# Optimization experiments

Measured on AMD Instinct MI355X. Metric: run time of the kernel, lower is better.

## Reference

```python
import jax, jax.numpy as jnp
import numpy as np

S, B, H, NH = 2048, 4, 1024, 16
HD = H // NH
MASK_VAL = -10000.0

def setup_inputs() -> dict:
    key = jax.random.key(0)
    ks = jax.random.split(key, 6)
    hidden_states = jax.random.normal(ks[0], (S, B, H), dtype=jnp.float32)
    attention_mask = jax.random.randint(ks[1], (B, 1, S, S), 0, 2).astype(bool)
    W_qkv = jax.random.normal(ks[2], (3 * H, H), dtype=jnp.float32) * (H ** -0.5)
    b_qkv = jax.random.normal(ks[3], (3 * H,), dtype=jnp.float32) * 0.02
    W_dense = jax.random.normal(ks[4], (H, H), dtype=jnp.float32) * (H ** -0.5)
    b_dense = jax.random.normal(ks[5], (H,), dtype=jnp.float32) * 0.02
    return {"hidden_states": hidden_states, "attention_mask": attention_mask,
            "W_qkv": W_qkv, "b_qkv": b_qkv, "W_dense": W_dense, "b_dense": b_dense}

def reference(hidden_states, attention_mask, W_qkv, b_qkv, W_dense, b_dense):
    # QKV projection: [s,b,h] -> [s,b,3h] -> [s,b,NH,3*HD], split last dim into q,k,v
    mixed = hidden_states @ W_qkv.T + b_qkv
    mixed = mixed.reshape(S, B, NH, 3 * HD)
    q, k, v = mixed[..., :HD], mixed[..., HD:2 * HD], mixed[..., 2 * HD:]
    norm_factor = jnp.float32(1.0 / np.sqrt(HD))
    # scores: [b, nh, sq, sk] (baddbmm beta=0.7 on torch.empty is undefined; baseline treated as 0)
    scores = jnp.einsum('sbhd,tbhd->bhst', q, k) * norm_factor
    scores = jnp.where(attention_mask, MASK_VAL, scores)
    probs = jax.nn.softmax(scores, axis=-1)
    # attention dropout (p=0.7) omitted for deterministic reference (eval mode)
    ctx = jnp.einsum('bhst,tbhd->sbhd', probs, v)  # [s,b,nh,hd]
    ctx = ctx.reshape(S, B, H)
    out = ctx @ W_dense.T + b_dense
    return out
```

## Files before the change

kernel.cpp:

```cpp
#include <hip/hip_runtime.h>
#include <hip/hip_bf16.h>
#include <math.h>

constexpr int S_ = 2048, B_ = 4, H_ = 1024, NH_ = 16, HD_ = 64;

typedef __attribute__((ext_vector_type(8))) short short8;
typedef __attribute__((ext_vector_type(4))) short short4v;
typedef __attribute__((ext_vector_type(4))) float floatx4;
typedef __attribute__((ext_vector_type(2))) unsigned uint2v;

static __device__ __forceinline__ short f2bf(float f) {
    union { float f; unsigned u; } v; v.f = f;
    unsigned r = v.u + 0x7FFFu + ((v.u >> 16) & 1u);
    return (short)(r >> 16);
}

static __device__ __forceinline__ unsigned pack_bf(float p0, float p1) {
    return __builtin_amdgcn_perm(__float_as_uint(p1), __float_as_uint(p0), 0x07060302u);
}
static __device__ __forceinline__ float bfl(unsigned u) { return __uint_as_float(u << 16); }
static __device__ __forceinline__ float bfh(unsigned u) { return __uint_as_float(u & 0xFFFF0000u); }

static __device__ __forceinline__ void gl2lds16(const void* g, void* l) {
    __builtin_amdgcn_global_load_lds(
        (const __attribute__((address_space(1))) void*)g,
        (__attribute__((address_space(3))) void*)l, 16, 0, 0);
}

static __device__ __forceinline__ short8 pswz(unsigned a0, unsigned a1,
                                              unsigned b0, unsigned b1) {
    uint2v r0 = __builtin_amdgcn_permlane32_swap(a0, b0, false, false);
    uint2v s0 = __builtin_amdgcn_permlane16_swap(r0.x, r0.y, false, false);
    uint2v r1 = __builtin_amdgcn_permlane32_swap(a1, b1, false, false);
    uint2v s1 = __builtin_amdgcn_permlane16_swap(r1.x, r1.y, false, false);
    union { unsigned u[4]; short8 s; } o;
    o.u[0] = s0.x;
    o.u[1] = s1.x;
    o.u[2] = s0.y;
    o.u[3] = s1.y;
    return o.s;
}

__global__ __launch_bounds__(256) void cvt3_kernel(
    const float* __restrict__ a, short* __restrict__ oa, int na,
    const float* __restrict__ b, short* __restrict__ ob, int nb,
    const float* __restrict__ c, short* __restrict__ oc, int nc)
{
    const int idx = blockIdx.x * 256 + threadIdx.x;
    const float* src; short* dst; int i;
    if (idx < na)            { src = a; dst = oa; i = idx; }
    else if (idx < na + nb)  { src = b; dst = ob; i = idx - na; }
    else                     { src = c; dst = oc; i = idx - na - nb; }
    const float4 v = ((const float4*)src)[i];
    short4v o = { (short)f2bf(v.x), (short)f2bf(v.y), (short)f2bf(v.z), (short)f2bf(v.w) };
    ((short4v*)dst)[i] = o;
}

__global__ __launch_bounds__(256) void mask_u8_kernel(
    const int* __restrict__ m, unsigned* __restrict__ mb)
{
    const int i = blockIdx.x * 256 + threadIdx.x;
    const int4 v = ((const int4*)m)[i];
    unsigned r = (v.x ? 0u : 0xFFu)      | (v.y ? 0u : 0xFF00u) |
                 (v.z ? 0u : 0xFF0000u)  | (v.w ? 0u : 0xFF000000u);
    mb[i] = r;
}

__global__ __launch_bounds__(256) void gemm_qkv_mfma(
    const short* __restrict__ A, const short* __restrict__ Bw,
    const float* __restrict__ bias,
    short* __restrict__ Qb, short* __restrict__ Kb, short* __restrict__ Vb)
{
    constexpr int K = H_;
    __shared__ __align__(16) short As[128 * 64];
    __shared__ __align__(16) short Bs[128 * 64];

    const int t = threadIdx.x;
    const int wave = t >> 6, lane = t & 63;
    const int l15 = lane & 15, quad = lane >> 4;
    const int wm = wave & 1, wn = wave >> 1;
    const int row0 = blockIdx.y * 128;
    const int col0 = blockIdx.x * 128;

    floatx4 acc[4][4];
#pragma unroll
    for (int mi = 0; mi < 4; ++mi)
#pragma unroll
        for (int ni = 0; ni < 4; ++ni)
            acc[mi][ni] = (floatx4){0.f, 0.f, 0.f, 0.f};

    for (int k0 = 0; k0 < K; k0 += 64) {
#pragma unroll
        for (int j = 0; j < 4; ++j) {
            const int c = wave * 256 + j * 64 + lane;
            const int r = c >> 3, jg = ((c & 7) ^ (r & 7)) * 8;
            gl2lds16(A  + (size_t)(row0 + r) * K + k0 + jg, &As[(wave * 256 + j * 64) * 8]);
            gl2lds16(Bw + (size_t)(col0 + r) * K + k0 + jg, &Bs[(wave * 256 + j * 64) * 8]);
        }
        __syncthreads();
#pragma unroll
        for (int kk = 0; kk < 64; kk += 32) {
            short8 af[4], bfr[4];
#pragma unroll
            for (int mi = 0; mi < 4; ++mi) {
                const int R = wm * 64 + mi * 16 + l15;
                af[mi] = *(const short8*)&As[R * 64 + ((((kk >> 3) + quad) ^ (R & 7)) * 8)];
            }
#pragma unroll
            for (int ni = 0; ni < 4; ++ni) {
                const int R = wn * 64 + ni * 16 + l15;
                bfr[ni] = *(const short8*)&Bs[R * 64 + ((((kk >> 3) + quad) ^ (R & 7)) * 8)];
            }
#pragma unroll
            for (int mi = 0; mi < 4; ++mi)
#pragma unroll
                for (int ni = 0; ni < 4; ++ni)
                    acc[mi][ni] = __builtin_amdgcn_mfma_f32_16x16x32_bf16(
                        af[mi], bfr[ni], acc[mi][ni], 0, 0, 0);
        }
        __syncthreads();
    }

#pragma unroll
    for (int ni = 0; ni < 4; ++ni) {
        const int gc = col0 + wn * 64 + ni * 16 + l15;
        const float bv = bias[gc];
        const int hh = gc / 192;
        const int rem = gc - hh * 192;
        const int which = rem >> 6, d = rem & 63;
#pragma unroll
        for (int mi = 0; mi < 4; ++mi)
#pragma unroll
            for (int i = 0; i < 4; ++i) {
                const int gr = row0 + wm * 64 + mi * 16 + quad * 4 + i;
                const int s = gr >> 2, bb = gr & 3;
                float fv = acc[mi][ni][i] + bv;
                const size_t ho = (size_t)(bb * NH_ + hh);
                if (which == 0)      Qb[(ho * S_ + s) * HD_ + d] = f2bf(fv * 0.1803368801111204f);
                else if (which == 1) Kb[(ho * S_ + s) * HD_ + d] = f2bf(fv);
                else                 Vb[(ho * S_ + s) * HD_ + d] = f2bf(fv);
            }
    }
}

__global__ __launch_bounds__(256) void vtrans_kernel(
    const short* __restrict__ Vb, short* __restrict__ Vtb)
{
    const int bh = blockIdx.y;
    const int s0 = blockIdx.x * 64;
    __shared__ __align__(16) short T[64 * 64];
    const int t = threadIdx.x;

#pragma unroll
    for (int it = 0; it < 2; ++it) {
        const int c = t + it * 256;
        const int r = c >> 3, jp = c & 7;
        const int jg = jp ^ ((r >> 3) & 7);
        *(short8*)&T[r * 64 + jp * 8] =
            *(const short8*)(Vb + ((size_t)bh * S_ + s0 + r) * HD_ + jg * 8);
    }
    __syncthreads();

#pragma unroll
    for (int it = 0; it < 2; ++it) {
        const int c = t + it * 256;
        const int d = c >> 3, sg = (c & 7) * 8;
        short8 v;
#pragma unroll
        for (int k = 0; k < 8; ++k) {
            const int r = sg + k;
            v[k] = T[r * 64 + (((d >> 3) ^ ((r >> 3) & 7)) * 8) + (d & 7)];
        }
        *(short8*)(Vtb + ((size_t)bh * HD_ + d) * S_ + s0 + sg) = v;
    }
}

__global__ __launch_bounds__(256) void gemm_dense_mfma(
    const short* __restrict__ A, const short* __restrict__ Bw,
    const float* __restrict__ bias, float* __restrict__ out)
{
    constexpr int K = H_;
    __shared__ __align__(16) short As[128 * 64];
    __shared__ __align__(16) short Bs[128 * 64];

    const int t = threadIdx.x;
    const int wave = t >> 6, lane = t & 63;
    const int l15 = lane & 15, quad = lane >> 4;
    const int wm = wave & 1, wn = wave >> 1;
    const int row0 = blockIdx.y * 128;
    const int col0 = blockIdx.x * 128;

    floatx4 acc[4][4];
#pragma unroll
    for (int mi = 0; mi < 4; ++mi)
#pragma unroll
        for (int ni = 0; ni < 4; ++ni)
            acc[mi][ni] = (floatx4){0.f, 0.f, 0.f, 0.f};

    for (int k0 = 0; k0 < K; k0 += 64) {
#pragma unroll
        for (int j = 0; j < 4; ++j) {
            const int c = wave * 256 + j * 64 + lane;
            const int r = c >> 3, jg = ((c & 7) ^ (r & 7)) * 8;
            gl2lds16(A  + (size_t)(row0 + r) * K + k0 + jg, &As[(wave * 256 + j * 64) * 8]);
            gl2lds16(Bw + (size_t)(col0 + r) * K + k0 + jg, &Bs[(wave * 256 + j * 64) * 8]);
        }
        __syncthreads();
#pragma unroll
        for (int kk = 0; kk < 64; kk += 32) {
            short8 af[4], bfr[4];
#pragma unroll
            for (int mi = 0; mi < 4; ++mi) {
                const int R = wm * 64 + mi * 16 + l15;
                af[mi] = *(const short8*)&As[R * 64 + ((((kk >> 3) + quad) ^ (R & 7)) * 8)];
            }
#pragma unroll
            for (int ni = 0; ni < 4; ++ni) {
                const int R = wn * 64 + ni * 16 + l15;
                bfr[ni] = *(const short8*)&Bs[R * 64 + ((((kk >> 3) + quad) ^ (R & 7)) * 8)];
            }
#pragma unroll
            for (int mi = 0; mi < 4; ++mi)
#pragma unroll
                for (int ni = 0; ni < 4; ++ni)
                    acc[mi][ni] = __builtin_amdgcn_mfma_f32_16x16x32_bf16(
                        af[mi], bfr[ni], acc[mi][ni], 0, 0, 0);
        }
        __syncthreads();
    }

#pragma unroll
    for (int ni = 0; ni < 4; ++ni) {
        const int gc = col0 + wn * 64 + ni * 16 + l15;
        const float bv = bias[gc];
#pragma unroll
        for (int mi = 0; mi < 4; ++mi)
#pragma unroll
            for (int i = 0; i < 4; ++i) {
                const int gr = row0 + wm * 64 + mi * 16 + quad * 4 + i;
                out[(size_t)gr * H_ + gc] = acc[mi][ni][i] + bv;
            }
    }
}

__global__ __launch_bounds__(256, 2) void flash_mfma_kernel(
    const short* __restrict__ Qb, const short* __restrict__ Kb,
    const short* __restrict__ Vtb, const unsigned char* __restrict__ mask8,
    short* __restrict__ ctxb)
{
    const int bh = blockIdx.y;
    const int b  = bh >> 4;
    const int h  = bh & 15;
    const int s0 = blockIdx.x * 256;

    const int tdx  = threadIdx.x;
    const int wave = tdx >> 6;
    const int lane = tdx & 63;
    const int l15  = lane & 15;
    const int quad = lane >> 4;

    __shared__ __align__(16) short Ks [3 * 4096];
    __shared__ __align__(16) short Vts[3 * 4096];

    const short* Qg = Qb + ((size_t)bh * S_ + s0 + wave * 64 + l15) * HD_;
    short8 qf[4][2];
#pragma unroll
    for (int g = 0; g < 4; ++g) {
        qf[g][0] = *(const short8*)(Qg + g * 16 * HD_ + quad * 8);
        qf[g][1] = *(const short8*)(Qg + g * 16 * HD_ + 32 + quad * 8);
    }

    const short* Kbase  = Kb  + (size_t)bh * S_ * HD_;
    const short* Vtbase = Vtb + (size_t)bh * HD_ * S_;
    const unsigned char* mr = mask8 + ((size_t)b * S_ + s0 + wave * 64 + l15) * S_ + quad * 4;

    floatx4 o[4][4];
    float ls[4] = {0.f, 0.f, 0.f, 0.f};
#pragma unroll
    for (int g = 0; g < 4; ++g)
#pragma unroll
        for (int n0 = 0; n0 < 4; ++n0) o[g][n0] = (floatx4){0.f, 0.f, 0.f, 0.f};

    const int cb0 = wave * 64, cb1 = (4 + wave) * 64;
    const int c0 = cb0 + lane,  c1 = cb1 + lane;
    const int r0 = c0 >> 3, jg0 = ((c0 & 7) ^ (r0 & 7)) * 8;
    const int r1 = c1 >> 3, jg1 = ((c1 & 7) ^ (r1 & 7)) * 8;

    gl2lds16(Kbase  + (size_t)r0 * HD_ + jg0, &Ks[cb0 * 8]);
    gl2lds16(Kbase  + (size_t)r1 * HD_ + jg1, &Ks[cb1 * 8]);
    gl2lds16(Vtbase + (size_t)r0 * S_ + jg0,  &Vts[cb0 * 8]);
    gl2lds16(Vtbase + (size_t)r1 * S_ + jg1,  &Vts[cb1 * 8]);
    __builtin_amdgcn_sched_barrier(0);
    gl2lds16(Kbase  + (size_t)(64 + r0) * HD_ + jg0, &Ks[4096 + cb0 * 8]);
    gl2lds16(Kbase  + (size_t)(64 + r1) * HD_ + jg1, &Ks[4096 + cb1 * 8]);
    gl2lds16(Vtbase + (size_t)r0 * S_ + 64 + jg0,    &Vts[4096 + cb0 * 8]);
    gl2lds16(Vtbase + (size_t)r1 * S_ + 64 + jg1,    &Vts[4096 + cb1 * 8]);
    __builtin_amdgcn_sched_barrier(0);
    unsigned mu[4][4], mun[4][4];
#pragma unroll
    for (int g = 0; g < 4; ++g)
#pragma unroll
        for (int n0 = 0; n0 < 4; ++n0)
            mu[g][n0] = *(const unsigned*)(mr + (size_t)g * 16 * S_ + n0 * 16);

    const floatx4 z4 = {0.f, 0.f, 0.f, 0.f};
    int boC = 0, boS = 2 * 4096;

#pragma unroll 1
    for (int it = 0; it < 32; ++it) {
        if (it < 31) { asm volatile("s_waitcnt vmcnt(20)" ::: "memory"); }
        else         { asm volatile("s_waitcnt vmcnt(16)" ::: "memory"); }
        __builtin_amdgcn_s_barrier();
        __builtin_amdgcn_sched_barrier(0);

        if (it < 30) {
            const size_t tn = (size_t)(it + 2) * 64;
            gl2lds16(Kbase  + (tn + r0) * HD_ + jg0,      &Ks[boS + cb0 * 8]);
            gl2lds16(Kbase  + (tn + r1) * HD_ + jg1,      &Ks[boS + cb1 * 8]);
            gl2lds16(Vtbase + (size_t)r0 * S_ + tn + jg0, &Vts[boS + cb0 * 8]);
            gl2lds16(Vtbase + (size_t)r1 * S_ + tn + jg1, &Vts[boS + cb1 * 8]);
        }
        __builtin_amdgcn_sched_barrier(0);
        if (it < 31) {
            const int tn1 = (it + 1) * 64;
#pragma unroll
            for (int g = 0; g < 4; ++g)
#pragma unroll
                for (int n0 = 0; n0 < 4; ++n0)
                    mun[g][n0] = *(const unsigned*)(mr + (size_t)g * 16 * S_ + tn1 + n0 * 16);
        }
        __builtin_amdgcn_sched_barrier(0);

#pragma unroll
        for (int h2 = 0; h2 < 2; ++h2) {
            unsigned uu[4][2][2];
            __builtin_amdgcn_s_setprio(1);
#pragma unroll
            for (int n0i = 0; n0i < 2; ++n0i) {
                const int n0 = h2 * 2 + n0i;
                const int R = n0 * 16 + l15, xr = R & 7;
                const short8 kb0 = *(const short8*)&Ks[boC + R * 64 + ((quad ^ xr) * 8)];
                const short8 kb1 = *(const short8*)&Ks[boC + R * 64 + (((quad + 4) ^ xr) * 8)];
#pragma unroll
                for (int g = 0; g < 4; ++g) {
                    floatx4 sc = __builtin_amdgcn_mfma_f32_16x16x32_bf16(kb0, qf[g][0], z4, 0, 0, 0);
                    sc = __builtin_amdgcn_mfma_f32_16x16x32_bf16(kb1, qf[g][1], sc, 0, 0, 0);
                    const unsigned q0 = __builtin_amdgcn_perm(0u, mu[g][n0], 0x01010000u);
                    const unsigned q1 = __builtin_amdgcn_perm(0u, mu[g][n0], 0x03030202u);
                    const unsigned u0 = pack_bf(__builtin_amdgcn_exp2f(sc[0]),
                                                __builtin_amdgcn_exp2f(sc[1])) & q0;
                    const unsigned u1 = pack_bf(__builtin_amdgcn_exp2f(sc[2]),
                                                __builtin_amdgcn_exp2f(sc[3])) & q1;
                    ls[g] += (bfl(u0) + bfh(u0)) + (bfl(u1) + bfh(u1));
                    uu[g][n0i][0] = u0; uu[g][n0i][1] = u1;
                }
            }
            __builtin_amdgcn_s_setprio(0);
            short8 pa[4];
#pragma unroll
            for (int g = 0; g < 4; ++g)
                pa[g] = pswz(uu[g][0][0], uu[g][0][1], uu[g][1][0], uu[g][1][1]);
            __builtin_amdgcn_s_setprio(1);
#pragma unroll
            for (int n0 = 0; n0 < 4; ++n0) {
                const int R = n0 * 16 + l15, xr = R & 7;
                const short8 vb = *(const short8*)&Vts[boC + R * 64 + (((quad + 4 * h2) ^ xr) * 8)];
#pragma unroll
                for (int g = 0; g < 4; ++g)
                    o[g][n0] = __builtin_amdgcn_mfma_f32_16x16x32_bf16(pa[g], vb, o[g][n0], 0, 0, 0);
            }
            __builtin_amdgcn_s_setprio(0);
        }

        boC = (boC == 2 * 4096) ? 0 : boC + 4096;
        boS = (boS == 2 * 4096) ? 0 : boS + 4096;
#pragma unroll
        for (int g = 0; g < 4; ++g)
#pragma unroll
            for (int n0 = 0; n0 < 4; ++n0) mu[g][n0] = mun[g][n0];
    }

#pragma unroll
    for (int g = 0; g < 4; ++g) {
        float lg = ls[g];
        lg += __shfl_xor(lg, 16);
        lg += __shfl_xor(lg, 32);
        const float li = 1.f / lg;
#pragma unroll
        for (int i = 0; i < 4; ++i) {
            const float la = __shfl(li, quad * 4 + i);
            const int sA = s0 + wave * 64 + g * 16 + quad * 4 + i;
#pragma unroll
            for (int n0 = 0; n0 < 4; ++n0)
                ctxb[((size_t)sA * B_ + b) * H_ + h * HD_ + n0 * 16 + l15] =
                    f2bf(o[g][n0][i] * la);
        }
    }
}

extern "C" void kernel_launch(void* const* d_in, const int* in_sizes, int n_in,
                              void* d_out, int out_size, void* d_ws, size_t ws_size,
                              hipStream_t stream)
{
    const float* hidden = (const float*)d_in[0];
    const int*   mask   = (const int*)d_in[1];
    const float* Wqkv   = (const float*)d_in[2];
    const float* bqkv   = (const float*)d_in[3];
    const float* Wd     = (const float*)d_in[4];
    const float* bd     = (const float*)d_in[5];
    float* out = (float*)d_out;

    const size_t HE = (size_t)B_ * NH_ * S_ * HD_;
    short* hBF    = (short*)d_ws;
    short* WqkvBF = hBF + (size_t)S_ * B_ * H_;
    short* WdBF   = WqkvBF + (size_t)3 * H_ * H_;
    short* Qb     = WdBF + (size_t)H_ * H_;
    short* Kb     = Qb + HE;
    short* Vb     = Kb + HE;
    short* Vtb    = Vb + HE;
    short* ctxb   = Vtb + HE;
    unsigned char* mask8 = (unsigned char*)hBF;

    const int nh4 = (S_ * B_ * H_) / 4;
    const int nw4 = (3 * H_ * H_) / 4;
    const int nd4 = (H_ * H_) / 4;
    hipLaunchKernelGGL(cvt3_kernel, dim3((nh4 + nw4 + nd4) / 256), dim3(256), 0, stream,
                       hidden, hBF, nh4, Wqkv, WqkvBF, nw4, Wd, WdBF, nd4);

    hipLaunchKernelGGL(gemm_qkv_mfma, dim3((3 * H_) / 128, (S_ * B_) / 128), dim3(256), 0, stream,
                       hBF, WqkvBF, bqkv, Qb, Kb, Vb);
    hipLaunchKernelGGL(mask_u8_kernel, dim3((B_ * S_ * S_ / 4) / 256), dim3(256), 0, stream,
                       mask, (unsigned*)mask8);
    hipLaunchKernelGGL(vtrans_kernel, dim3(S_ / 64, B_ * NH_), dim3(256), 0, stream,
                       Vb, Vtb);
    hipLaunchKernelGGL(flash_mfma_kernel, dim3(S_ / 256, B_ * NH_), dim3(256), 0, stream,
                       Qb, Kb, Vtb, mask8, ctxb);
    hipLaunchKernelGGL(gemm_dense_mfma, dim3(H_ / 128, (S_ * B_) / 128), dim3(256), 0, stream,
                       ctxb, WdBF, bd, out);
}
```

Before: 404.4 us.

## Halve flash-attention query tile per block and double-buffer mask registers

The flash attention kernel now processes 128 query rows per block (32 per wave) instead of 256, doubling the grid to 1024 blocks and raising the launch-bounds occupancy target to 3 blocks per CU. The inner loop is restructured to compute all QK scores for a 64-key tile before exp/pack, and to use a full 64-wide K in the PV MFMAs. The loop is unrolled by two with ping-pong mask registers, which replaces the register copy, and the last tile is peeled. The aim is to fill CUs better and cut register pressure, at the cost of reloading K/V tiles from memory twice as often per query row.

```diff
diff --git a/kernel.cpp b/kernel.cpp
--- a/kernel.cpp
+++ b/kernel.cpp
@@ -243,7 +243,7 @@
     }
 }
 
-__global__ __launch_bounds__(256, 2) void flash_mfma_kernel(
+__global__ __launch_bounds__(256, 3) void flash_mfma_kernel(
     const short* __restrict__ Qb, const short* __restrict__ Kb,
     const short* __restrict__ Vtb, const unsigned char* __restrict__ mask8,
     short* __restrict__ ctxb)
@@ -251,7 +251,7 @@
     const int bh = blockIdx.y;
     const int b  = bh >> 4;
     const int h  = bh & 15;
-    const int s0 = blockIdx.x * 256;
+    const int s0 = blockIdx.x * 128;
 
     const int tdx  = threadIdx.x;
     const int wave = tdx >> 6;
@@ -262,22 +262,22 @@
     __shared__ __align__(16) short Ks [3 * 4096];
     __shared__ __align__(16) short Vts[3 * 4096];
 
-    const short* Qg = Qb + ((size_t)bh * S_ + s0 + wave * 64 + l15) * HD_;
-    short8 qf[4][2];
-#pragma unroll
-    for (int g = 0; g < 4; ++g) {
+    const short* Qg = Qb + ((size_t)bh * S_ + s0 + wave * 32 + l15) * HD_;
+    short8 qf[2][2];
+#pragma unroll
+    for (int g = 0; g < 2; ++g) {
         qf[g][0] = *(const short8*)(Qg + g * 16 * HD_ + quad * 8);
         qf[g][1] = *(const short8*)(Qg + g * 16 * HD_ + 32 + quad * 8);
     }
 
     const short* Kbase  = Kb  + (size_t)bh * S_ * HD_;
     const short* Vtbase = Vtb + (size_t)bh * HD_ * S_;
-    const unsigned char* mr = mask8 + ((size_t)b * S_ + s0 + wave * 64 + l15) * S_ + quad * 4;
-
-    floatx4 o[4][4];
-    float ls[4] = {0.f, 0.f, 0.f, 0.f};
-#pragma unroll
-    for (int g = 0; g < 4; ++g)
+    const unsigned char* mr = mask8 + ((size_t)b * S_ + s0 + wave * 32 + l15) * S_ + quad * 4;
+
+    floatx4 o[2][4];
+    float ls[2] = {0.f, 0.f};
+#pragma unroll
+    for (int g = 0; g < 2; ++g)
 #pragma unroll
         for (int n0 = 0; n0 < 4; ++n0) o[g][n0] = (floatx4){0.f, 0.f, 0.f, 0.f};
 
@@ -285,6 +285,8 @@
     const int c0 = cb0 + lane,  c1 = cb1 + lane;
     const int r0 = c0 >> 3, jg0 = ((c0 & 7) ^ (r0 & 7)) * 8;
     const int r1 = c1 >> 3, jg1 = ((c1 & 7) ^ (r1 & 7)) * 8;
+
+    unsigned muA[2][4], muB[2][4];
 
     gl2lds16(Kbase  + (size_t)r0 * HD_ + jg0, &Ks[cb0 * 8]);
     gl2lds16(Kbase  + (size_t)r1 * HD_ + jg1, &Ks[cb1 * 8]);
@@ -296,23 +298,67 @@
     gl2lds16(Vtbase + (size_t)r0 * S_ + 64 + jg0,    &Vts[4096 + cb0 * 8]);
     gl2lds16(Vtbase + (size_t)r1 * S_ + 64 + jg1,    &Vts[4096 + cb1 * 8]);
     __builtin_amdgcn_sched_barrier(0);
-    unsigned mu[4][4], mun[4][4];
-#pragma unroll
-    for (int g = 0; g < 4; ++g)
+#pragma unroll
+    for (int g = 0; g < 2; ++g)
 #pragma unroll
         for (int n0 = 0; n0 < 4; ++n0)
-            mu[g][n0] = *(const unsigned*)(mr + (size_t)g * 16 * S_ + n0 * 16);
+            muA[g][n0] = *(const unsigned*)(mr + (size_t)g * 16 * S_ + n0 * 16);
 
     const floatx4 z4 = {0.f, 0.f, 0.f, 0.f};
     int boC = 0, boS = 2 * 4096;
 
-#pragma unroll 1
-    for (int it = 0; it < 32; ++it) {
-        if (it < 31) { asm volatile("s_waitcnt vmcnt(20)" ::: "memory"); }
-        else         { asm volatile("s_waitcnt vmcnt(16)" ::: "memory"); }
+    auto compute_tile = [&](const unsigned (&mc)[2][4]) {
+        floatx4 sc[2][4];
+        __builtin_amdgcn_s_setprio(1);
+#pragma unroll
+        for (int n0 = 0; n0 < 4; ++n0) {
+            const int R = n0 * 16 + l15, xr = R & 7;
+            const short8 kb0 = *(const short8*)&Ks[boC + R * 64 + ((quad ^ xr) * 8)];
+            const short8 kb1 = *(const short8*)&Ks[boC + R * 64 + (((quad + 4) ^ xr) * 8)];
+            sc[0][n0] = __builtin_amdgcn_mfma_f32_16x16x32_bf16(kb0, qf[0][0], z4, 0, 0, 0);
+            sc[0][n0] = __builtin_amdgcn_mfma_f32_16x16x32_bf16(kb1, qf[0][1], sc[0][n0], 0, 0, 0);
+            sc[1][n0] = __builtin_amdgcn_mfma_f32_16x16x32_bf16(kb0, qf[1][0], z4, 0, 0, 0);
+            sc[1][n0] = __builtin_amdgcn_mfma_f32_16x16x32_bf16(kb1, qf[1][1], sc[1][n0], 0, 0, 0);
+        }
+        __builtin_amdgcn_s_setprio(0);
+        unsigned uu[2][4][2];
+#pragma unroll
+        for (int g = 0; g < 2; ++g)
+#pragma unroll
+            for (int n0 = 0; n0 < 4; ++n0) {
+                const floatx4 v = sc[g][n0];
+                const unsigned q0 = __builtin_amdgcn_perm(0u, mc[g][n0], 0x01010000u);
+                const unsigned q1 = __builtin_amdgcn_perm(0u, mc[g][n0], 0x03030202u);
+                const unsigned u0 = pack_bf(__builtin_amdgcn_exp2f(v[0]),
+                                            __builtin_amdgcn_exp2f(v[1])) & q0;
+                const unsigned u1 = pack_bf(__builtin_amdgcn_exp2f(v[2]),
+                                            __builtin_amdgcn_exp2f(v[3])) & q1;
+                ls[g] += (bfl(u0) + bfh(u0)) + (bfl(u1) + bfh(u1));
+                uu[g][n0][0] = u0; uu[g][n0][1] = u1;
+            }
+        short8 pa[2][2];
+        pa[0][0] = pswz(uu[0][0][0], uu[0][0][1], uu[0][1][0], uu[0][1][1]);
+        pa[0][1] = pswz(uu[0][2][0], uu[0][2][1], uu[0][3][0], uu[0][3][1]);
+        pa[1][0] = pswz(uu[1][0][0], uu[1][0][1], uu[1][1][0], uu[1][1][1]);
+        pa[1][1] = pswz(uu[1][2][0], uu[1][2][1], uu[1][3][0], uu[1][3][1]);
+        __builtin_amdgcn_s_setprio(1);
+#pragma unroll
+        for (int n0 = 0; n0 < 4; ++n0) {
+            const int R = n0 * 16 + l15, xr = R & 7;
+            const short8 vb0 = *(const short8*)&Vts[boC + R * 64 + ((quad ^ xr) * 8)];
+            const short8 vb1 = *(const short8*)&Vts[boC + R * 64 + (((quad + 4) ^ xr) * 8)];
+            o[0][n0] = __builtin_amdgcn_mfma_f32_16x16x32_bf16(pa[0][0], vb0, o[0][n0], 0, 0, 0);
+            o[0][n0] = __builtin_amdgcn_mfma_f32_16x16x32_bf16(pa[0][1], vb1, o[0][n0], 0, 0, 0);
+            o[1][n0] = __builtin_amdgcn_mfma_f32_16x16x32_bf16(pa[1][0], vb0, o[1][n0], 0, 0, 0);
+            o[1][n0] = __builtin_amdgcn_mfma_f32_16x16x32_bf16(pa[1][1], vb1, o[1][n0], 0, 0, 0);
+        }
+        __builtin_amdgcn_s_setprio(0);
+    };
+
+    auto body = [&](int it, const unsigned (&mc)[2][4], unsigned (&mn)[2][4]) {
+        asm volatile("s_waitcnt vmcnt(12)" ::: "memory");
         __builtin_amdgcn_s_barrier();
         __builtin_amdgcn_sched_barrier(0);
-
         if (it < 30) {
             const size_t tn = (size_t)(it + 2) * 64;
             gl2lds16(Kbase  + (tn + r0) * HD_ + jg0,      &Ks[boS + cb0 * 8]);
@@ -321,67 +367,33 @@
             gl2lds16(Vtbase + (size_t)r1 * S_ + tn + jg1, &Vts[boS + cb1 * 8]);
         }
         __builtin_amdgcn_sched_barrier(0);
-        if (it < 31) {
+        {
             const int tn1 = (it + 1) * 64;
 #pragma unroll
-            for (int g = 0; g < 4; ++g)
+            for (int g = 0; g < 2; ++g)
 #pragma unroll
                 for (int n0 = 0; n0 < 4; ++n0)
-                    mun[g][n0] = *(const unsigned*)(mr + (size_t)g * 16 * S_ + tn1 + n0 * 16);
+                    mn[g][n0] = *(const unsigned*)(mr + (size_t)g * 16 * S_ + tn1 + n0 * 16);
         }
         __builtin_amdgcn_sched_barrier(0);
-
-#pragma unroll
-        for (int h2 = 0; h2 < 2; ++h2) {
-            unsigned uu[4][2][2];
-            __builtin_amdgcn_s_setprio(1);
-#pragma unroll
-            for (int n0i = 0; n0i < 2; ++n0i) {
-                const int n0 = h2 * 2 + n0i;
-                const int R = n0 * 16 + l15, xr = R & 7;
-                const short8 kb0 = *(const short8*)&Ks[boC + R * 64 + ((quad ^ xr) * 8)];
-                const short8 kb1 = *(const short8*)&Ks[boC + R * 64 + (((quad + 4) ^ xr) * 8)];
-#pragma unroll
-                for (int g = 0; g < 4; ++g) {
-                    floatx4 sc = __builtin_amdgcn_mfma_f32_16x16x32_bf16(kb0, qf[g][0], z4, 0, 0, 0);
-                    sc = __builtin_amdgcn_mfma_f32_16x16x32_bf16(kb1, qf[g][1], sc, 0, 0, 0);
-                    const unsigned q0 = __builtin_amdgcn_perm(0u, mu[g][n0], 0x01010000u);
-                    const unsigned q1 = __builtin_amdgcn_perm(0u, mu[g][n0], 0x03030202u);
-                    const unsigned u0 = pack_bf(__builtin_amdgcn_exp2f(sc[0]),
-                                                __builtin_amdgcn_exp2f(sc[1])) & q0;
-                    const unsigned u1 = pack_bf(__builtin_amdgcn_exp2f(sc[2]),
-                                                __builtin_amdgcn_exp2f(sc[3])) & q1;
-                    ls[g] += (bfl(u0) + bfh(u0)) + (bfl(u1) + bfh(u1));
-                    uu[g][n0i][0] = u0; uu[g][n0i][1] = u1;
-                }
-            }
-            __builtin_amdgcn_s_setprio(0);
-            short8 pa[4];
-#pragma unroll
-            for (int g = 0; g < 4; ++g)
-                pa[g] = pswz(uu[g][0][0], uu[g][0][1], uu[g][1][0], uu[g][1][1]);
-            __builtin_amdgcn_s_setprio(1);
-#pragma unroll
-            for (int n0 = 0; n0 < 4; ++n0) {
-                const int R = n0 * 16 + l15, xr = R & 7;
-                const short8 vb = *(const short8*)&Vts[boC + R * 64 + (((quad + 4 * h2) ^ xr) * 8)];
-#pragma unroll
-                for (int g = 0; g < 4; ++g)
-                    o[g][n0] = __builtin_amdgcn_mfma_f32_16x16x32_bf16(pa[g], vb, o[g][n0], 0, 0, 0);
-            }
-            __builtin_amdgcn_s_setprio(0);
-        }
-
+        compute_tile(mc);
         boC = (boC == 2 * 4096) ? 0 : boC + 4096;
         boS = (boS == 2 * 4096) ? 0 : boS + 4096;
-#pragma unroll
-        for (int g = 0; g < 4; ++g)
-#pragma unroll
-            for (int n0 = 0; n0 < 4; ++n0) mu[g][n0] = mun[g][n0];
-    }
-
-#pragma unroll
-    for (int g = 0; g < 4; ++g) {
+    };
+
+#pragma unroll 1
+    for (int it = 0; it < 30; it += 2) {
+        body(it,     muA, muB);
+        body(it + 1, muB, muA);
+    }
+    body(30, muA, muB);
+    asm volatile("s_waitcnt vmcnt(8)" ::: "memory");
+    __builtin_amdgcn_s_barrier();
+    __builtin_amdgcn_sched_barrier(0);
+    compute_tile(muB);
+
+#pragma unroll
+    for (int g = 0; g < 2; ++g) {
         float lg = ls[g];
         lg += __shfl_xor(lg, 16);
         lg += __shfl_xor(lg, 32);
@@ -389,7 +401,7 @@
 #pragma unroll
         for (int i = 0; i < 4; ++i) {
             const float la = __shfl(li, quad * 4 + i);
-            const int sA = s0 + wave * 64 + g * 16 + quad * 4 + i;
+            const int sA = s0 + wave * 32 + g * 16 + quad * 4 + i;
 #pragma unroll
             for (int n0 = 0; n0 < 4; ++n0)
                 ctxb[((size_t)sA * B_ + b) * H_ + h * HD_ + n0 * 16 + l15] =
@@ -433,7 +445,7 @@
                        mask, (unsigned*)mask8);
     hipLaunchKernelGGL(vtrans_kernel, dim3(S_ / 64, B_ * NH_), dim3(256), 0, stream,
                        Vb, Vtb);
-    hipLaunchKernelGGL(flash_mfma_kernel, dim3(S_ / 256, B_ * NH_), dim3(256), 0, stream,
+    hipLaunchKernelGGL(flash_mfma_kernel, dim3(S_ / 128, B_ * NH_), dim3(256), 0, stream,
                        Qb, Kb, Vtb, mask8, ctxb);
     hipLaunchKernelGGL(gemm_dense_mfma, dim3(H_ / 128, (S_ * B_) / 128), dim3(256), 0, stream,
                        ctxb, WdBF, bd, out);
```

Result: slower. 439.9 us (+8.8%).
